# Performance work log

Hardware: AMD Instinct MI355X
Metric: run time of the kernel (lower is better)

Reference implementation:

```python
import math
import jax, jax.numpy as jnp
import numpy as np

B, T, D = 4, 2048, 768
NH, DH = 12, 64

def setup_inputs() -> dict:
    key = jax.random.key(0)
    k1, k2, k3 = jax.random.split(key, 3)
    scale_attn = 1.0 / math.sqrt(D)
    scale_proj = 1.0 / math.sqrt(D)
    return {
        "x": jax.random.normal(k1, (B, T, D), dtype=jnp.float32),
        "w_attn": jax.random.normal(k2, (D, 3 * D), dtype=jnp.float32) * scale_attn,
        "b_attn": jnp.zeros((3 * D,), dtype=jnp.float32),
        "w_proj": jax.random.normal(k3, (D, D), dtype=jnp.float32) * scale_proj,
        "b_proj": jnp.zeros((D,), dtype=jnp.float32),
    }

def reference(x, w_attn, b_attn, w_proj, b_proj):
    Bx, Tx, Dx = x.shape
    qkv = x @ w_attn + b_attn                     # [B, T, 3D]
    q, k, v = jnp.split(qkv, 3, axis=-1)          # each [B, T, D]
    # [B, T, D] -> [B, NH, T, DH]
    def to_heads(t):
        return t.reshape(Bx, Tx, NH, DH).transpose(0, 2, 1, 3)
    q, k, v = to_heads(q), to_heads(k), to_heads(v)
    attn = jnp.einsum("bhqd,bhkd->bhqk", q, k) / math.sqrt(DH)
    causal = jnp.tril(jnp.ones((Tx, Tx), dtype=bool))
    attn = jnp.where(causal[None, None, :, :], attn, -jnp.inf)
    attn = jax.nn.softmax(attn, axis=-1)
    out = jnp.einsum("bhqk,bhkd->bhqd", attn, v)  # [B, NH, T, DH]
    out = out.transpose(0, 2, 1, 3).reshape(Bx, Tx, Dx)
    out = out @ w_proj + b_proj
    return (out, (k, v))
```

## Files before the change

kernel.cpp:

```cpp
#include <hip/hip_runtime.h>
#include <hip/hip_bf16.h>

typedef unsigned short ushort_t;
typedef __attribute__((ext_vector_type(8))) short short8;
typedef __attribute__((ext_vector_type(4))) float f32x4;

#define B_    4
#define T_    2048
#define D_    768
#define NH_   12
#define DH_   64
#define KDIM  768

__device__ __forceinline__ ushort_t f2bf(float f) {
  union { float f; unsigned u; } c; c.f = f;
  unsigned u = c.u;
  return (ushort_t)((u + 0x7FFFu + ((u >> 16) & 1u)) >> 16);
}

__device__ __forceinline__ unsigned cvt_pk_bf16(float lo, float hi) {
  unsigned r;
  asm("v_cvt_pk_bf16_f32 %0, %1, %2" : "=v"(r) : "v"(lo), "v"(hi));
  return r;
}

__device__ __forceinline__ void gload_lds16(const void* g, void* l) {
  __builtin_amdgcn_global_load_lds(
      (const __attribute__((address_space(1))) unsigned int*)g,
      (__attribute__((address_space(3))) unsigned int*)l, 16, 0, 0);
}

__global__ void cvt_bf16_vec(const float* __restrict__ in,
                             ushort_t* __restrict__ out, int n4) {
  int i = blockIdx.x * blockDim.x + threadIdx.x;
  if (i >= n4) return;
  float4 v = ((const float4*)in)[i];
  ushort4 o;
  o.x = f2bf(v.x); o.y = f2bf(v.y); o.z = f2bf(v.z); o.w = f2bf(v.w);
  ((ushort4*)out)[i] = o;
}

__global__ void transpose_cvt(const float* __restrict__ in,
                              ushort_t* __restrict__ out, int R, int C) {
  __shared__ float tile[32][33];
  int c0 = blockIdx.x * 32, r0 = blockIdx.y * 32;
  int tx = threadIdx.x, ty = threadIdx.y;
#pragma unroll
  for (int j = 0; j < 32; j += 8)
    tile[ty + j][tx] = in[(size_t)(r0 + ty + j) * C + c0 + tx];
  __syncthreads();
#pragma unroll
  for (int j = 0; j < 32; j += 8)
    out[(size_t)(c0 + ty + j) * R + r0 + tx] = f2bf(tile[tx][ty + j]);
}

__device__ __forceinline__ void gemm128_mainloop(
    const ushort_t* __restrict__ A, const ushort_t* __restrict__ BT,
    int m0, int n0, ushort_t* lds, f32x4 acc[4][4]) {
  const int t = threadIdx.x;
  const int l = t & 63;
  const int w = t >> 6;
  const int wm = w >> 1, wn = w & 1;
  const int c0 = t, c1 = t + 256;
  const ushort_t* ga0 = A + (size_t)(m0 + (c0 >> 2)) * KDIM + ((c0 & 3) << 3);
  const ushort_t* ga1 = A + (size_t)(m0 + (c1 >> 2)) * KDIM + ((c1 & 3) << 3);
  const ushort_t* gb0 = BT + (size_t)(n0 + (c0 >> 2)) * KDIM + ((c0 & 3) << 3);
  const ushort_t* gb1 = BT + (size_t)(n0 + (c1 >> 2)) * KDIM + ((c1 & 3) << 3);
  ushort_t* la0 = lds + (0 * 256 + w * 64) * 8;
  ushort_t* la1 = lds + (1 * 256 + w * 64) * 8;
  ushort_t* lb0 = lds + 4096 + (0 * 256 + w * 64) * 8;
  ushort_t* lb1 = lds + 4096 + (1 * 256 + w * 64) * 8;
  const int frag_off = ((l & 15) * 32) + ((l >> 4) * 8);

  for (int k0 = 0; k0 < KDIM; k0 += 32) {
    gload_lds16(ga0 + k0, la0);
    gload_lds16(ga1 + k0, la1);
    gload_lds16(gb0 + k0, lb0);
    gload_lds16(gb1 + k0, lb1);
    __syncthreads();
    short8 af[4], bfv[4];
#pragma unroll
    for (int mt = 0; mt < 4; ++mt)
      af[mt] = *(const short8*)&lds[(wm * 64 + mt * 16) * 32 + frag_off];
#pragma unroll
    for (int nt = 0; nt < 4; ++nt)
      bfv[nt] = *(const short8*)&lds[4096 + (wn * 64 + nt * 16) * 32 + frag_off];
#pragma unroll
    for (int mt = 0; mt < 4; ++mt)
#pragma unroll
      for (int nt = 0; nt < 4; ++nt)
        acc[mt][nt] = __builtin_amdgcn_mfma_f32_16x16x32_bf16(
            af[mt], bfv[nt], acc[mt][nt], 0, 0, 0);
    __syncthreads();
  }
}

__global__ __launch_bounds__(256) void gemm_qkv_kernel(
    const ushort_t* __restrict__ xbf, const ushort_t* __restrict__ wT,
    const float* __restrict__ bias, ushort_t* __restrict__ qbf,
    float* __restrict__ kout, float* __restrict__ vout,
    ushort_t* __restrict__ kbf, ushort_t* __restrict__ vtbf) {
  __shared__ ushort_t lds[8192];
  int bid = blockIdx.x;
  int m0 = (bid & 63) << 7;
  int n0 = (bid >> 6) << 7;
  f32x4 acc[4][4];
  f32x4 zero = {0.f, 0.f, 0.f, 0.f};
#pragma unroll
  for (int a = 0; a < 4; ++a)
#pragma unroll
    for (int b = 0; b < 4; ++b) acc[a][b] = zero;
  gemm128_mainloop(xbf, wT, m0, n0, lds, acc);

  const float QSC = 0.125f * 1.44269504089f;
  const int l = threadIdx.x & 63, w = threadIdx.x >> 6;
  const int wm = w >> 1, wn = w & 1;
  const int sec = n0 / 768;
  const int b = m0 >> 11;
  const int tt_base = (m0 & 2047) + wm * 64;
#pragma unroll
  for (int nt = 0; nt < 4; ++nt) {
    int n = n0 + wn * 64 + nt * 16 + (l & 15);
    float bv = bias[n];
    int nn = n - sec * 768;
    int h = nn >> 6, dh = nn & 63;
    size_t head_base = ((size_t)(b * NH_ + h) * T_);
#pragma unroll
    for (int mt = 0; mt < 4; ++mt) {
      int tt0 = tt_base + mt * 16 + ((l >> 4) << 2);
      float vals[4];
#pragma unroll
      for (int r = 0; r < 4; ++r) vals[r] = acc[mt][nt][r] + bv;
      if (sec == 0) {
#pragma unroll
        for (int r = 0; r < 4; ++r)
          qbf[((head_base + tt0 + r) << 6) + dh] = f2bf(vals[r] * QSC);
      } else if (sec == 1) {
#pragma unroll
        for (int r = 0; r < 4; ++r) {
          size_t idx = ((head_base + tt0 + r) << 6) + dh;
          kout[idx] = vals[r];
          kbf[idx] = f2bf(vals[r]);
        }
      } else {
#pragma unroll
        for (int r = 0; r < 4; ++r)
          vout[((head_base + tt0 + r) << 6) + dh] = vals[r];
        ushort4 pk;
        pk.x = f2bf(vals[0]); pk.y = f2bf(vals[1]);
        pk.z = f2bf(vals[2]); pk.w = f2bf(vals[3]);
        *(ushort4*)&vtbf[((size_t)(b * NH_ + h) * DH_ + dh) * T_ + tt0] = pk;
      }
    }
  }
}

__global__ __launch_bounds__(256) void gemm_proj_kernel(
    const ushort_t* __restrict__ abf, const ushort_t* __restrict__ wT,
    const float* __restrict__ bias, float* __restrict__ out) {
  __shared__ ushort_t lds[8192];
  int bid = blockIdx.x;
  int m0 = (bid & 63) << 7;
  int n0 = (bid >> 6) << 7;
  f32x4 acc[4][4];
  f32x4 zero = {0.f, 0.f, 0.f, 0.f};
#pragma unroll
  for (int a = 0; a < 4; ++a)
#pragma unroll
    for (int b = 0; b < 4; ++b) acc[a][b] = zero;
  gemm128_mainloop(abf, wT, m0, n0, lds, acc);

  const int l = threadIdx.x & 63, w = threadIdx.x >> 6;
  const int wm = w >> 1, wn = w & 1;
#pragma unroll
  for (int nt = 0; nt < 4; ++nt) {
    int n = n0 + wn * 64 + nt * 16 + (l & 15);
    float bv = bias[n];
#pragma unroll
    for (int mt = 0; mt < 4; ++mt) {
#pragma unroll
      for (int r = 0; r < 4; ++r) {
        int m = m0 + wm * 64 + mt * 16 + ((l >> 4) << 2) + r;
        out[(size_t)m * D_ + n] = acc[mt][nt][r] + bv;
      }
    }
  }
}

__device__ __forceinline__ void strip_exp_store(
    f32x4 s4[4], int gq, bool diag, int kvb, int g, int qi, char* pbase) {
  if (diag) {
#pragma unroll
    for (int nt = 0; nt < 4; ++nt)
#pragma unroll
      for (int r = 0; r < 4; ++r) {
        int gk = kvb + nt * 16 + g * 4 + r;
        if (gk > gq) s4[nt][r] = -1e30f;
      }
  }
#pragma unroll
  for (int nt = 0; nt < 4; ++nt) {
    float p0 = exp2f(s4[nt][0]);
    float p1 = exp2f(s4[nt][1]);
    float p2 = exp2f(s4[nt][2]);
    float p3 = exp2f(s4[nt][3]);
    uint2 pk;
    pk.x = cvt_pk_bf16(p0, p1);
    pk.y = cvt_pk_bf16(p2, p3);
    *(uint2*)(pbase + ((nt * 32 + g * 8) ^ ((qi & 7) << 4))) = pk;
  }
}

__global__ __launch_bounds__(512, 6) void attn_fwd_kernel(
    const ushort_t* __restrict__ qbf, const ushort_t* __restrict__ kbf,
    const ushort_t* __restrict__ vtbf, ushort_t* __restrict__ obf) {
  __shared__ ushort_t Kl[2][4096];
  __shared__ ushort_t Vt[2][4096];
  __shared__ ushort_t Pl[8][1024];
  const int bid = blockIdx.x;
  const int swz = (bid & 7) * 96 + (bid >> 3);
  const int jp = swz & 15;
  const int bh = swz >> 4;
  const int qlo = jp << 6, qhi = (31 - jp) << 6;
  const int lastH = 31 - jp, lastL = jp;
  const int t = threadIdx.x, l = t & 63, w = t >> 6;
  const int g = l >> 4, qi = l & 15;
  const bool isHi = (w < 4);
  const int wc = isHi ? w : (w - 4);
  const int qs0 = (isHi ? qhi : qlo) + wc * 16;
  const int lastMe = isHi ? lastH : lastL;

  const ushort_t* Qb = qbf + (size_t)bh * T_ * DH_;
  const ushort_t* Kb = kbf + (size_t)bh * T_ * DH_;
  const ushort_t* Vb = vtbf + (size_t)bh * DH_ * T_;

  const int row0 = t >> 3, ch0 = t & 7;
  const ushort_t* gK0 = Kb + row0 * DH_ + ((ch0 ^ (row0 & 7)) << 3);
  const ushort_t* gV0 = Vb + (size_t)row0 * T_ + ((ch0 ^ (row0 & 7)) << 3);

  short8 aq[2];
  {
    const int qr = qs0 + qi;
    aq[0] = *(const short8*)&Qb[(size_t)qr * DH_ + (g << 3)];
    aq[1] = *(const short8*)&Qb[(size_t)qr * DH_ + (g << 3) + 32];
  }

  short8 ones;
#pragma unroll
  for (int j = 0; j < 8; ++j) ones[j] = (short)0x3F80;

  f32x4 o[4], al;
  f32x4 zero = {0.f, 0.f, 0.f, 0.f};
#pragma unroll
  for (int nt = 0; nt < 4; ++nt) o[nt] = zero;
  al = zero;

  gload_lds16(gK0, &Kl[0][w * 512]);
  gload_lds16(gV0, &Vt[0][w * 512]);

  char* pb = (char*)&Pl[w][0] + qi * 128;

  for (int kt = 0; kt <= lastH; ++kt) {
    const int buf = kt & 1;
    const int kvb = kt << 6;
    asm volatile("s_waitcnt vmcnt(0)" ::: "memory");
    __builtin_amdgcn_sched_barrier(0);
    __builtin_amdgcn_s_barrier();
    __builtin_amdgcn_sched_barrier(0);
    if (kt < lastH) {
      const int nx = kt + 1;
      gload_lds16(gK0 + (size_t)nx * 4096, &Kl[buf ^ 1][w * 512]);
      gload_lds16(gV0 + (size_t)nx * 64, &Vt[buf ^ 1][w * 512]);
    }
    if (kt <= lastMe) {
      f32x4 s4[4];
#pragma unroll
      for (int nt = 0; nt < 4; ++nt) s4[nt] = zero;
#pragma unroll
      for (int h2 = 0; h2 < 2; ++h2) {
#pragma unroll
        for (int nt = 0; nt < 4; ++nt) {
          short8 bk = *(const short8*)&Kl[buf][((nt * 16 + qi) << 6) +
                                              (((g + 4 * h2) ^ (qi & 7)) << 3)];
          s4[nt] = __builtin_amdgcn_mfma_f32_16x16x32_bf16(bk, aq[h2],
                                                           s4[nt], 0, 0, 0);
        }
      }
      strip_exp_store(s4, qs0 + qi, kt == lastMe, kvb, g, qi, pb);
#pragma unroll
      for (int k2 = 0; k2 < 2; ++k2) {
        short8 pf = *(const short8*)(pb + ((g * 16 + k2 * 64) ^ ((qi & 7) << 4)));
#pragma unroll
        for (int nt = 0; nt < 4; ++nt) {
          short8 av = *(const short8*)&Vt[buf][((nt * 16 + qi) << 6) +
                                               (((g + 4 * k2) ^ (qi & 7)) << 3)];
          o[nt] = __builtin_amdgcn_mfma_f32_16x16x32_bf16(av, pf, o[nt],
                                                          0, 0, 0);
        }
        al = __builtin_amdgcn_mfma_f32_16x16x32_bf16(ones, pf, al, 0, 0, 0);
      }
    }
  }

  const int b = bh / NH_, h = bh - b * NH_;
  {
    float inv = 1.f / al[0];
    int q = qs0 + qi;
    size_t rowb = (size_t)(b * T_ + q) * D_ + h * DH_;
#pragma unroll
    for (int nt = 0; nt < 4; ++nt) {
      ushort4 pk;
      pk.x = f2bf(o[nt][0] * inv);
      pk.y = f2bf(o[nt][1] * inv);
      pk.z = f2bf(o[nt][2] * inv);
      pk.w = f2bf(o[nt][3] * inv);
      *(ushort4*)&obf[rowb + nt * 16 + g * 4] = pk;
    }
  }
}

extern "C" void kernel_launch(void* const* d_in, const int* in_sizes, int n_in,
                              void* d_out, int out_size, void* d_ws, size_t ws_size,
                              hipStream_t stream) {
  const float* x      = (const float*)d_in[0];
  const float* w_attn = (const float*)d_in[1];
  const float* b_attn = (const float*)d_in[2];
  const float* w_proj = (const float*)d_in[3];
  const float* b_proj = (const float*)d_in[4];

  float* out  = (float*)d_out;
  float* kout = out + (size_t)B_ * T_ * D_;
  float* vout = kout + (size_t)B_ * T_ * D_;

  char* ws = (char*)d_ws;
  ushort_t* xbf = (ushort_t*)(ws);
  ushort_t* wTa = (ushort_t*)(ws + 12582912);
  ushort_t* wTp = (ushort_t*)(ws + 16121856);
  ushort_t* qbf = (ushort_t*)(ws + 17301504);
  ushort_t* kbf = (ushort_t*)(ws + 29884416);
  ushort_t* vtbf = (ushort_t*)(ws + 42467328);
  ushort_t* abf = xbf;

  cvt_bf16_vec<<<6144, 256, 0, stream>>>(x, xbf, (B_ * T_ * D_) / 4);
  dim3 tb(32, 8);
  transpose_cvt<<<dim3(72, 24), tb, 0, stream>>>(w_attn, wTa, D_, 3 * D_);
  transpose_cvt<<<dim3(24, 24), tb, 0, stream>>>(w_proj, wTp, D_, D_);

  gemm_qkv_kernel<<<64 * 18, 256, 0, stream>>>(xbf, wTa, b_attn, qbf, kout, vout,
                                               kbf, vtbf);
  attn_fwd_kernel<<<768, 512, 0, stream>>>(qbf, kbf, vtbf, abf);
  gemm_proj_kernel<<<64 * 6, 256, 0, stream>>>(abf, wTp, b_proj, out);
}
```

Before: 140.1 us.

## Double-buffer GEMM LDS tiles and XOR-swizzle fragment layout

Changes the shared GEMM mainloop used by the QKV and projection kernels to double-buffer LDS. The next K-slice's global-to-LDS loads are issued right after the barrier, so they overlap the current slice's MFMAs, and one of the two barriers per iteration is removed. It also applies an XOR swizzle on 16-byte chunks, on both the global source column and the fragment read offset, to reduce LDS bank conflicts. LDS usage per block doubles, which may lower occupancy; the attention kernel is untouched, so the gain is limited to the GEMM share of total time.

```diff
diff --git a/kernel.cpp b/kernel.cpp
--- a/kernel.cpp
+++ b/kernel.cpp
@@ -61,37 +61,50 @@
   const int l = t & 63;
   const int w = t >> 6;
   const int wm = w >> 1, wn = w & 1;
+  const int g = l >> 4, qi = l & 15;
   const int c0 = t, c1 = t + 256;
-  const ushort_t* ga0 = A + (size_t)(m0 + (c0 >> 2)) * KDIM + ((c0 & 3) << 3);
-  const ushort_t* ga1 = A + (size_t)(m0 + (c1 >> 2)) * KDIM + ((c1 & 3) << 3);
-  const ushort_t* gb0 = BT + (size_t)(n0 + (c0 >> 2)) * KDIM + ((c0 & 3) << 3);
-  const ushort_t* gb1 = BT + (size_t)(n0 + (c1 >> 2)) * KDIM + ((c1 & 3) << 3);
-  ushort_t* la0 = lds + (0 * 256 + w * 64) * 8;
-  ushort_t* la1 = lds + (1 * 256 + w * 64) * 8;
-  ushort_t* lb0 = lds + 4096 + (0 * 256 + w * 64) * 8;
-  ushort_t* lb1 = lds + 4096 + (1 * 256 + w * 64) * 8;
-  const int frag_off = ((l & 15) * 32) + ((l >> 4) * 8);
-
-  for (int k0 = 0; k0 < KDIM; k0 += 32) {
-    gload_lds16(ga0 + k0, la0);
-    gload_lds16(ga1 + k0, la1);
-    gload_lds16(gb0 + k0, lb0);
-    gload_lds16(gb1 + k0, lb1);
-    __syncthreads();
+  const int r0 = c0 >> 2, r1 = c1 >> 2;
+  const int s0 = (c0 & 3) ^ ((r0 >> 2) & 3);
+  const int s1 = (c1 & 3) ^ ((r1 >> 2) & 3);
+  const ushort_t* ga0 = A + (size_t)(m0 + r0) * KDIM + (s0 << 3);
+  const ushort_t* ga1 = A + (size_t)(m0 + r1) * KDIM + (s1 << 3);
+  const ushort_t* gb0 = BT + (size_t)(n0 + r0) * KDIM + (s0 << 3);
+  const ushort_t* gb1 = BT + (size_t)(n0 + r1) * KDIM + (s1 << 3);
+  const int NK = KDIM / 32;
+  const int rsw = (g ^ qi >> 2) << 3;
+
+  gload_lds16(ga0, lds + w * 512);
+  gload_lds16(ga1, lds + 2048 + w * 512);
+  gload_lds16(gb0, lds + 4096 + w * 512);
+  gload_lds16(gb1, lds + 6144 + w * 512);
+
+  for (int kk = 0; kk < NK; ++kk) {
+    asm volatile("s_waitcnt vmcnt(0)" ::: "memory");
+    __builtin_amdgcn_sched_barrier(0);
+    __builtin_amdgcn_s_barrier();
+    __builtin_amdgcn_sched_barrier(0);
+    if (kk + 1 < NK) {
+      ushort_t* ln = lds + ((kk + 1) & 1) * 8192;
+      int k0 = (kk + 1) * 32;
+      gload_lds16(ga0 + k0, ln + w * 512);
+      gload_lds16(ga1 + k0, ln + 2048 + w * 512);
+      gload_lds16(gb0 + k0, ln + 4096 + w * 512);
+      gload_lds16(gb1 + k0, ln + 6144 + w * 512);
+    }
+    ushort_t* lb = lds + (kk & 1) * 8192;
     short8 af[4], bfv[4];
 #pragma unroll
     for (int mt = 0; mt < 4; ++mt)
-      af[mt] = *(const short8*)&lds[(wm * 64 + mt * 16) * 32 + frag_off];
+      af[mt] = *(const short8*)&lb[(wm * 64 + mt * 16 + qi) * 32 + rsw];
 #pragma unroll
     for (int nt = 0; nt < 4; ++nt)
-      bfv[nt] = *(const short8*)&lds[4096 + (wn * 64 + nt * 16) * 32 + frag_off];
+      bfv[nt] = *(const short8*)&lb[4096 + (wn * 64 + nt * 16 + qi) * 32 + rsw];
 #pragma unroll
     for (int mt = 0; mt < 4; ++mt)
 #pragma unroll
       for (int nt = 0; nt < 4; ++nt)
         acc[mt][nt] = __builtin_amdgcn_mfma_f32_16x16x32_bf16(
             af[mt], bfv[nt], acc[mt][nt], 0, 0, 0);
-    __syncthreads();
   }
 }
 
@@ -100,7 +113,7 @@
     const float* __restrict__ bias, ushort_t* __restrict__ qbf,
     float* __restrict__ kout, float* __restrict__ vout,
     ushort_t* __restrict__ kbf, ushort_t* __restrict__ vtbf) {
-  __shared__ ushort_t lds[8192];
+  __shared__ ushort_t lds[16384];
   int bid = blockIdx.x;
   int m0 = (bid & 63) << 7;
   int n0 = (bid >> 6) << 7;
@@ -158,7 +171,7 @@
 __global__ __launch_bounds__(256) void gemm_proj_kernel(
     const ushort_t* __restrict__ abf, const ushort_t* __restrict__ wT,
     const float* __restrict__ bias, float* __restrict__ out) {
-  __shared__ ushort_t lds[8192];
+  __shared__ ushort_t lds[16384];
   int bid = blockIdx.x;
   int m0 = (bid & 63) << 7;
   int n0 = (bid >> 6) << 7;
```

Result: no change. 140.6 us (+0.4%).
